# Kernel tuning notes

Hardware: AMD Instinct MI355X
Metric: run time of the kernel (lower is better)

## Reference

```python
import jax, jax.numpy as jnp
import numpy as np

EMB = 768
HEADS = 8
HEAD_DIM = EMB // HEADS  # 96
SCALING = HEAD_DIM ** -0.5


def setup_inputs() -> dict:
    key = jax.random.key(0)
    ks = jax.random.split(key, 9)
    B, S = 2, 2048
    std = 1.0 / np.sqrt(EMB)
    x = jax.random.normal(ks[0], (B, S, EMB), dtype=jnp.float32)
    # torch nn.Linear weights are [out, in]; we store [in, out] for x @ W.
    Wq = jax.random.normal(ks[1], (EMB, EMB), dtype=jnp.float32) * std
    Wk = jax.random.normal(ks[2], (EMB, EMB), dtype=jnp.float32) * std
    Wv = jax.random.normal(ks[3], (EMB, EMB), dtype=jnp.float32) * std
    Wo = jax.random.normal(ks[4], (EMB, EMB), dtype=jnp.float32) * std
    bq = jax.random.normal(ks[5], (EMB,), dtype=jnp.float32) * std
    bk = jax.random.normal(ks[6], (EMB,), dtype=jnp.float32) * std
    bv = jax.random.normal(ks[7], (EMB,), dtype=jnp.float32) * std
    bo = jax.random.normal(ks[8], (EMB,), dtype=jnp.float32) * std
    return {"x": x, "Wq": Wq, "bq": bq, "Wk": Wk, "bk": bk,
            "Wv": Wv, "bv": bv, "Wo": Wo, "bo": bo}


def _split_heads(t):
    # [B, S, E] -> [B, H, S, D]
    B, S, _ = t.shape
    return t.reshape(B, S, HEADS, HEAD_DIM).transpose(0, 2, 1, 3)


def reference(x, Wq, bq, Wk, bk, Wv, bv, Wo, bo):
    q = _split_heads(x @ Wq + bq)
    k = _split_heads(x @ Wk + bk)
    v = _split_heads(x @ Wv + bv)
    # Full [B, H, S, S] score matrix, as in the source module.
    energies = jnp.einsum('bhqd,bhkd->bhqk', q, k)
    # Faithful quirk: softmax first, THEN multiply by scaling (dropout=0 -> identity).
    attention = jax.nn.softmax(energies, axis=-1) * SCALING
    out = jnp.einsum('bhqk,bhkd->bhqd', attention, v)
    B, H, S, D = out.shape
    out = out.transpose(0, 2, 1, 3).reshape(B, S, H * D)
    return out @ Wo + bo
```

## Files before the change

### kernel.cpp

```cpp
#include <hip/hip_runtime.h>
#include <hip/hip_bf16.h>

#define EMB 768
#define HD 96
#define NH 8
#define SEQ 2048
#define SCALING 0.10206207261596575f

typedef short bf16x8 __attribute__((ext_vector_type(8)));
typedef float f32x4  __attribute__((ext_vector_type(4)));
typedef unsigned short u16v8 __attribute__((ext_vector_type(8)));
typedef unsigned short u16v4 __attribute__((ext_vector_type(4)));

union F4 { float4 v; float f[4]; };

__device__ __forceinline__ unsigned short f2bf(float v) {
    __hip_bfloat16 b = __float2bfloat16(v);
    return *reinterpret_cast<unsigned short*>(&b);
}
__device__ __forceinline__ float bf2f(unsigned short u) {
    __hip_bfloat16 b = *reinterpret_cast<__hip_bfloat16*>(&u);
    return __bfloat162float(b);
}

__device__ __forceinline__ void dma16(const unsigned short* g, unsigned short* l) {
    __builtin_amdgcn_global_load_lds(
        (const __attribute__((address_space(1))) unsigned int*)g,
        (__attribute__((address_space(3))) unsigned int*)l,
        16, 0, 0);
}

__global__ __launch_bounds__(256) void convert_x(
    const float* __restrict__ x,
    unsigned short* __restrict__ xh, unsigned short* __restrict__ xl)
{
    const size_t i0 = ((size_t)blockIdx.x * 256 + threadIdx.x) * 8;
    F4 a, b;
    a.v = *(const float4*)&x[i0];
    b.v = *(const float4*)&x[i0 + 4];
    u16v8 h, l;
    #pragma unroll
    for (int j = 0; j < 4; j++) {
        unsigned short hu = f2bf(a.f[j]);
        h[j] = hu; l[j] = f2bf(a.f[j] - bf2f(hu));
    }
    #pragma unroll
    for (int j = 0; j < 4; j++) {
        unsigned short hu = f2bf(b.f[j]);
        h[4+j] = hu; l[4+j] = f2bf(b.f[j] - bf2f(hu));
    }
    *(u16v8*)&xh[i0] = h;
    *(u16v8*)&xl[i0] = l;
}

__global__ __launch_bounds__(256) void convert_wT(
    const float* __restrict__ Wq, const float* __restrict__ Wk,
    const float* __restrict__ Wv, const float* __restrict__ Wo,
    unsigned short* __restrict__ WhT, unsigned short* __restrict__ WlT)
{
    const int z = blockIdx.z;
    const float* W = (z == 0) ? Wq : (z == 1) ? Wk : (z == 2) ? Wv : Wo;
    unsigned short* oh = WhT + (size_t)z * 589824;
    unsigned short* ol = WlT + (size_t)z * 589824;
    __shared__ float T[64][68];
    const int t = threadIdx.x;
    const int r = t >> 2, cg = (t & 3) * 16;
    const int k0 = blockIdx.x * 64, n0 = blockIdx.y * 64;
    #pragma unroll
    for (int i = 0; i < 4; i++) {
        float4 v = *(const float4*)&W[(size_t)(k0 + r) * EMB + n0 + cg + 4*i];
        *(float4*)&T[r][cg + 4*i] = v;
    }
    __syncthreads();
    #pragma unroll
    for (int i = 0; i < 4; i++) {
        u16v4 h, l;
        #pragma unroll
        for (int j = 0; j < 4; j++) {
            float v = T[cg + 4*i + j][r];
            unsigned short hu = f2bf(v);
            h[j] = hu; l[j] = f2bf(v - bf2f(hu));
        }
        *(u16v4*)&oh[(size_t)(n0 + r) * EMB + k0 + cg + 4*i] = h;
        *(u16v4*)&ol[(size_t)(n0 + r) * EMB + k0 + cg + 4*i] = l;
    }
}

#define QA_H 0
#define QA_L 4096
#define QW_H 8192
#define QW_L 12288

__global__ __launch_bounds__(256, 3) void qkv_mfma(
    const unsigned short* __restrict__ xh, const unsigned short* __restrict__ xl,
    const unsigned short* __restrict__ WhT, const unsigned short* __restrict__ WlT,
    const float* __restrict__ bq, const float* __restrict__ bk, const float* __restrict__ bv,
    unsigned short* __restrict__ Qh, unsigned short* __restrict__ Ql,
    unsigned short* __restrict__ Kb, unsigned short* __restrict__ Vt)
{
    const int which = blockIdx.z;
    const unsigned short* Wh = WhT + (size_t)which * 589824;
    const unsigned short* Wl = WlT + (size_t)which * 589824;
    const float* bias = (which == 0) ? bq : (which == 1) ? bk : bv;

    __shared__ __align__(16) unsigned short lds[16384];
    const int tid = threadIdx.x;
    const int lane = tid & 63, lo = lane & 15, h4 = lane >> 4;
    const int w = tid >> 6, wm = w & 1, wn = w >> 1;
    const int row0 = blockIdx.x * 128, col0 = blockIdx.y * 128;

    const unsigned short* sbase =
        (w == 0) ? xh + (size_t)row0 * EMB :
        (w == 1) ? xl + (size_t)row0 * EMB :
        (w == 2) ? Wh + (size_t)col0 * EMB :
                   Wl + (size_t)col0 * EMB;
    const int soff = w * 4096;

    f32x4 acc[4][4];
    #pragma unroll
    for (int i = 0; i < 4; i++)
        #pragma unroll
        for (int j = 0; j < 4; j++) acc[i][j] = (f32x4){0.f, 0.f, 0.f, 0.f};

    for (int k0 = 0; k0 < EMB; k0 += 32) {
        #pragma unroll
        for (int j = 0; j < 8; j++) {
            const int u = j*64 + lane;
            const int row = u >> 2, c8 = (u & 3) * 8;
            dma16(sbase + (size_t)row * EMB + k0 + c8, &lds[soff + j*512]);
        }
        __syncthreads();

        bf16x8 ah[4], al[4];
        #pragma unroll
        for (int i = 0; i < 4; i++)
            ah[i] = *(const bf16x8*)&lds[QA_H + (64*wm + 16*i + lo)*32 + 8*h4];
        if (which <= 1) {
            #pragma unroll
            for (int i = 0; i < 4; i++)
                al[i] = *(const bf16x8*)&lds[QA_L + (64*wm + 16*i + lo)*32 + 8*h4];
        }
        #pragma unroll
        for (int j = 0; j < 4; j++) {
            bf16x8 whf = *(const bf16x8*)&lds[QW_H + (64*wn + 16*j + lo)*32 + 8*h4];
            #pragma unroll
            for (int i = 0; i < 4; i++)
                acc[i][j] = __builtin_amdgcn_mfma_f32_16x16x32_bf16(ah[i], whf, acc[i][j], 0, 0, 0);
            if (which <= 1) {
                #pragma unroll
                for (int i = 0; i < 4; i++)
                    acc[i][j] = __builtin_amdgcn_mfma_f32_16x16x32_bf16(al[i], whf, acc[i][j], 0, 0, 0);
            }
            if (which != 1) {
                bf16x8 wlf = *(const bf16x8*)&lds[QW_L + (64*wn + 16*j + lo)*32 + 8*h4];
                #pragma unroll
                for (int i = 0; i < 4; i++)
                    acc[i][j] = __builtin_amdgcn_mfma_f32_16x16x32_bf16(ah[i], wlf, acc[i][j], 0, 0, 0);
            }
        }
        __syncthreads();
    }

    if (which == 0) {
        #pragma unroll
        for (int i = 0; i < 4; i++)
            #pragma unroll
            for (int r = 0; r < 4; r++) {
                const int sg = row0 + 64*wm + 16*i + 4*h4 + r;
                const int b = sg >> 11, s = sg & 2047;
                #pragma unroll
                for (int j = 0; j < 4; j++) {
                    const int c = col0 + 64*wn + 16*j + lo;
                    const int h = c / HD, d = c - h*HD;
                    float v = acc[i][j][r] + bias[c];
                    unsigned short hu = f2bf(v);
                    const size_t base = ((size_t)(b*NH + h) * SEQ + s) * HD + d;
                    Qh[base] = hu;
                    Ql[base] = f2bf(v - bf2f(hu));
                }
            }
    } else if (which == 1) {
        #pragma unroll
        for (int i = 0; i < 4; i++)
            #pragma unroll
            for (int r = 0; r < 4; r++) {
                const int sg = row0 + 64*wm + 16*i + 4*h4 + r;
                const int b = sg >> 11, s = sg & 2047;
                #pragma unroll
                for (int j = 0; j < 4; j++) {
                    const int c = col0 + 64*wn + 16*j + lo;
                    const int h = c / HD, d = c - h*HD;
                    float v = acc[i][j][r] + bias[c];
                    Kb[((size_t)(b*NH + h) * SEQ + s) * HD + d] = f2bf(v);
                }
            }
    } else {
        #pragma unroll
        for (int i = 0; i < 4; i++)
            #pragma unroll
            for (int r = 0; r < 4; r++) {
                const int sg = row0 + 64*wm + 16*i + 4*h4 + r;
                const int b = sg >> 11, s = sg & 2047;
                #pragma unroll
                for (int j = 0; j < 4; j++) {
                    const int c = col0 + 64*wn + 16*j + lo;
                    const int h = c / HD, d = c - h*HD;
                    float v = acc[i][j][r] + bias[c];
                    Vt[((size_t)(b*NH + h) * HD + d) * SEQ + s] = f2bf(v);
                }
            }
    }
}

#define PA_O 0
#define PWH_O 4096
#define PWL_O 6144

__global__ __launch_bounds__(256, 3) void proj_mfma(
    const unsigned short* __restrict__ AOh,
    const unsigned short* __restrict__ Wh, const unsigned short* __restrict__ Wl,
    const float* __restrict__ bo, float* __restrict__ out)
{
    __shared__ __align__(16) unsigned short lds[8192];
    const int tid = threadIdx.x;
    const int lane = tid & 63, lo = lane & 15, h4 = lane >> 4;
    const int w = tid >> 6, wm = w & 1, wn = w >> 1;
    const int row0 = blockIdx.x * 128, col0 = blockIdx.y * 64;

    const unsigned short* sbase =
        (w <= 1) ? AOh + (size_t)row0 * EMB :
        (w == 2) ? Wh  + (size_t)col0 * EMB :
                   Wl  + (size_t)col0 * EMB;
    const int jbase = (w == 1) ? 4 : 0;
    const int soff  = (w <= 1) ? PA_O : (w == 2) ? PWH_O : PWL_O;

    f32x4 acc[4][2];
    #pragma unroll
    for (int i = 0; i < 4; i++)
        #pragma unroll
        for (int j = 0; j < 2; j++) acc[i][j] = (f32x4){0.f, 0.f, 0.f, 0.f};

    for (int k0 = 0; k0 < EMB; k0 += 32) {
        #pragma unroll
        for (int jj = 0; jj < 4; jj++) {
            const int j = jbase + jj;
            const int u = j*64 + lane;
            const int row = u >> 2, c8 = (u & 3) * 8;
            dma16(sbase + (size_t)row * EMB + k0 + c8, &lds[soff + j*512]);
        }
        __syncthreads();

        bf16x8 af[4];
        #pragma unroll
        for (int i = 0; i < 4; i++)
            af[i] = *(const bf16x8*)&lds[PA_O + (64*wm + 16*i + lo)*32 + 8*h4];
        #pragma unroll
        for (int j = 0; j < 2; j++) {
            bf16x8 whf = *(const bf16x8*)&lds[PWH_O + (32*wn + 16*j + lo)*32 + 8*h4];
            bf16x8 wlf = *(const bf16x8*)&lds[PWL_O + (32*wn + 16*j + lo)*32 + 8*h4];
            #pragma unroll
            for (int i = 0; i < 4; i++) {
                acc[i][j] = __builtin_amdgcn_mfma_f32_16x16x32_bf16(af[i], whf, acc[i][j], 0, 0, 0);
                acc[i][j] = __builtin_amdgcn_mfma_f32_16x16x32_bf16(af[i], wlf, acc[i][j], 0, 0, 0);
            }
        }
        __syncthreads();
    }

    #pragma unroll
    for (int i = 0; i < 4; i++)
        #pragma unroll
        for (int r = 0; r < 4; r++) {
            const int sg = row0 + 64*wm + 16*i + 4*h4 + r;
            #pragma unroll
            for (int j = 0; j < 2; j++) {
                const int c = col0 + 32*wn + 16*j + lo;
                out[(size_t)sg * EMB + c] = acc[i][j][r] + bo[c];
            }
        }
}

__global__ __launch_bounds__(128, 2) void attn_mfma(
    const unsigned short* __restrict__ Qh, const unsigned short* __restrict__ Ql,
    const unsigned short* __restrict__ Kb, const unsigned short* __restrict__ Vt,
    unsigned short* __restrict__ AOh)
{
    __shared__ __align__(16) unsigned short lds[11072];
    const int id   = blockIdx.x;
    const int bh   = 2*(id & 7) + ((id >> 3) & 1);
    const int qb   = id >> 4;
    const int q0   = qb * 32;
    const int tid  = threadIdx.x;
    const int wk   = tid >> 6;
    const int lane = tid & 63;
    const int lo   = lane & 15;
    const int h4   = lane >> 4;

    bf16x8 qhf[2][3], qlf[2][3];
    #pragma unroll
    for (int mi = 0; mi < 2; mi++) {
        const size_t qoff = ((size_t)bh*SEQ + q0 + 16*mi + lo) * HD + 8*h4;
        #pragma unroll
        for (int ks = 0; ks < 3; ks++) {
            qhf[mi][ks] = *(const bf16x8*)&Qh[qoff + 32*ks];
            qlf[mi][ks] = *(const bf16x8*)&Ql[qoff + 32*ks];
        }
    }

    f32x4 O[2][6];
    #pragma unroll
    for (int mi = 0; mi < 2; mi++)
        #pragma unroll
        for (int i = 0; i < 6; i++) O[mi][i] = (f32x4){0.f, 0.f, 0.f, 0.f};
    float lsum[2][4] = {};

    unsigned short* Pw = lds + wk * 2304;
    const unsigned short* KbH = Kb + (size_t)bh * SEQ * HD;
    const unsigned short* VtH = Vt + (size_t)bh * HD * SEQ;

    #pragma unroll 1
    for (int c = 0; c < 16; c++) {
        const int k0 = (wk * 16 + c) * 64;
        const unsigned short* KbG = KbH + (size_t)k0 * HD;
        const unsigned short* VtG = VtH + k0;

        bf16x8 vf[2][6];
        #pragma unroll
        for (int ks2 = 0; ks2 < 2; ks2++)
            #pragma unroll
            for (int nb2 = 0; nb2 < 6; nb2++)
                vf[ks2][nb2] = *(const bf16x8*)&VtG[(size_t)(16*nb2 + lo)*SEQ + 32*ks2 + 8*h4];

        f32x4 S[2][4];
        #pragma unroll
        for (int mi = 0; mi < 2; mi++)
            #pragma unroll
            for (int nb = 0; nb < 4; nb++) S[mi][nb] = (f32x4){0.f, 0.f, 0.f, 0.f};
        #pragma unroll
        for (int ks = 0; ks < 3; ks++) {
            bf16x8 kf[4];
            #pragma unroll
            for (int nb = 0; nb < 4; nb++)
                kf[nb] = *(const bf16x8*)&KbG[(size_t)(16*nb + lo)*HD + 32*ks + 8*h4];
            #pragma unroll
            for (int nb = 0; nb < 4; nb++)
                #pragma unroll
                for (int mi = 0; mi < 2; mi++) {
                    S[mi][nb] = __builtin_amdgcn_mfma_f32_16x16x32_bf16(qhf[mi][ks], kf[nb], S[mi][nb], 0, 0, 0);
                    S[mi][nb] = __builtin_amdgcn_mfma_f32_16x16x32_bf16(qlf[mi][ks], kf[nb], S[mi][nb], 0, 0, 0);
                }
        }

        #pragma unroll
        for (int mi = 0; mi < 2; mi++)
            #pragma unroll
            for (int nb = 0; nb < 4; nb++)
                #pragma unroll
                for (int r = 0; r < 4; r++) {
                    float p = __expf(S[mi][nb][r]);
                    lsum[mi][r] += p;
                    Pw[(16*mi + 4*h4 + r)*72 + 16*nb + lo] = f2bf(p);
                }

        #pragma unroll
        for (int ks2 = 0; ks2 < 2; ks2++) {
            bf16x8 pf0 = *(const bf16x8*)&Pw[(lo)*72      + 32*ks2 + 8*h4];
            bf16x8 pf1 = *(const bf16x8*)&Pw[(16 + lo)*72 + 32*ks2 + 8*h4];
            #pragma unroll
            for (int nb2 = 0; nb2 < 6; nb2++) {
                O[0][nb2] = __builtin_amdgcn_mfma_f32_16x16x32_bf16(pf0, vf[ks2][nb2], O[0][nb2], 0, 0, 0);
                O[1][nb2] = __builtin_amdgcn_mfma_f32_16x16x32_bf16(pf1, vf[ks2][nb2], O[1][nb2], 0, 0, 0);
            }
        }
    }

    float lred[2][4];
    #pragma unroll
    for (int mi = 0; mi < 2; mi++)
        #pragma unroll
        for (int r = 0; r < 4; r++) {
            float l = lsum[mi][r];
            l += __shfl_xor(l, 1);
            l += __shfl_xor(l, 2);
            l += __shfl_xor(l, 4);
            l += __shfl_xor(l, 8);
            lred[mi][r] = l;
        }

    float* Cbuf = (float*)(lds + 4608);
    float* Lbuf = Cbuf + 3200;
    if (wk == 1) {
        #pragma unroll
        for (int mi = 0; mi < 2; mi++)
            #pragma unroll
            for (int r = 0; r < 4; r++) {
                const int row = 16*mi + 4*h4 + r;
                if (lo == 0) Lbuf[row] = lred[mi][r];
                #pragma unroll
                for (int nb2 = 0; nb2 < 6; nb2++)
                    Cbuf[row*100 + 16*nb2 + lo] = O[mi][nb2][r];
            }
    }
    __syncthreads();
    if (wk == 0) {
        const int b = bh >> 3, hh = bh & 7;
        #pragma unroll
        for (int mi = 0; mi < 2; mi++)
            #pragma unroll
            for (int r = 0; r < 4; r++) {
                const int row = 16*mi + 4*h4 + r;
                const float lt = lred[mi][r] + Lbuf[row];
                const float sc = SCALING / lt;
                const int q = q0 + row;
                const size_t base = ((size_t)b*SEQ + q)*EMB + hh*HD + lo;
                #pragma unroll
                for (int nb2 = 0; nb2 < 6; nb2++)
                    AOh[base + 16*nb2] =
                        f2bf((O[mi][nb2][r] + Cbuf[row*100 + 16*nb2 + lo]) * sc);
            }
    }
}

extern "C" void kernel_launch(void* const* d_in, const int* in_sizes, int n_in,
                              void* d_out, int out_size, void* d_ws, size_t ws_size,
                              hipStream_t stream)
{
    const float* x  = (const float*)d_in[0];
    const float* Wq = (const float*)d_in[1];
    const float* bq = (const float*)d_in[2];
    const float* Wk = (const float*)d_in[3];
    const float* bk = (const float*)d_in[4];
    const float* Wv = (const float*)d_in[5];
    const float* bv = (const float*)d_in[6];
    const float* Wo = (const float*)d_in[7];
    const float* bo = (const float*)d_in[8];
    float* out = (float*)d_out;

    unsigned short* ws = (unsigned short*)d_ws;
    const size_t HS = (size_t)16 * SEQ * HD;
    const size_t WS1 = (size_t)EMB * EMB;
    unsigned short* Qh  = ws;
    unsigned short* Ql  = ws + HS;
    unsigned short* Kb  = ws + 2*HS;
    unsigned short* Vt  = ws + 3*HS;
    unsigned short* xh  = ws + 4*HS;
    unsigned short* xl  = ws + 5*HS;
    unsigned short* WhT = ws + 6*HS;
    unsigned short* WlT = ws + 6*HS + 4*WS1;
    unsigned short* AOh = xh;

    convert_x<<<1536, 256, 0, stream>>>(x, xh, xl);
    convert_wT<<<dim3(12, 12, 4), 256, 0, stream>>>(Wq, Wk, Wv, Wo, WhT, WlT);
    qkv_mfma<<<dim3(32, 6, 3), 256, 0, stream>>>(xh, xl, WhT, WlT, bq, bk, bv,
                                                 Qh, Ql, Kb, Vt);
    attn_mfma<<<1024, 128, 0, stream>>>(Qh, Ql, Kb, Vt, AOh);
    proj_mfma<<<dim3(32, 12), 256, 0, stream>>>(AOh, WhT + 3*WS1, WlT + 3*WS1, bo, out);
}
```

Baseline: 235.4 us.

## Share K/V tiles across four query warps via double-buffered LDS staging

The attention kernel changes from 128-thread blocks of 32 queries with the key range split between two warps to 256-thread blocks where four warps each own 32 queries and sweep all keys. K and V^T tiles are staged cooperatively into padded, double-buffered LDS, with register prefetch of the next tile, instead of each warp loading its own fragments from global memory. Global K/V traffic per query drops about fourfold and the cross-warp reduction in the epilogue goes away. In exchange the grid shrinks from 1024 to 256 blocks, which is exactly one block per CU at about 72KB LDS each, and a barrier is added per key tile.

```diff
diff --git a/kernel.cpp b/kernel.cpp
--- a/kernel.cpp
+++ b/kernel.cpp
@@ -280,18 +280,24 @@
         }
 }
 
-__global__ __launch_bounds__(128, 2) void attn_mfma(
+#define AKB0 0
+#define AVB0 6656
+#define ABUF 13568
+#define AP_OFF 27136
+
+__global__ __launch_bounds__(256, 1) void attn_mfma(
     const unsigned short* __restrict__ Qh, const unsigned short* __restrict__ Ql,
     const unsigned short* __restrict__ Kb, const unsigned short* __restrict__ Vt,
     unsigned short* __restrict__ AOh)
 {
-    __shared__ __align__(16) unsigned short lds[11072];
+    __shared__ __align__(16) unsigned short lds[36352];
     const int id   = blockIdx.x;
-    const int bh   = 2*(id & 7) + ((id >> 3) & 1);
-    const int qb   = id >> 4;
-    const int q0   = qb * 32;
+    const int xcd  = id & 7;
+    const int j    = id >> 3;
+    const int bh   = 2*xcd + (j & 1);
+    const int q0   = (j >> 1) * 128;
     const int tid  = threadIdx.x;
-    const int wk   = tid >> 6;
+    const int w    = tid >> 6;
     const int lane = tid & 63;
     const int lo   = lane & 15;
     const int h4   = lane >> 4;
@@ -299,7 +305,7 @@
     bf16x8 qhf[2][3], qlf[2][3];
     #pragma unroll
     for (int mi = 0; mi < 2; mi++) {
-        const size_t qoff = ((size_t)bh*SEQ + q0 + 16*mi + lo) * HD + 8*h4;
+        const size_t qoff = ((size_t)bh*SEQ + q0 + 32*w + 16*mi + lo) * HD + 8*h4;
         #pragma unroll
         for (int ks = 0; ks < 3; ks++) {
             qhf[mi][ks] = *(const bf16x8*)&Qh[qoff + 32*ks];
@@ -314,22 +320,41 @@
         for (int i = 0; i < 6; i++) O[mi][i] = (f32x4){0.f, 0.f, 0.f, 0.f};
     float lsum[2][4] = {};
 
-    unsigned short* Pw = lds + wk * 2304;
+    unsigned short* Pw = lds + AP_OFF + w * 2304;
     const unsigned short* KbH = Kb + (size_t)bh * SEQ * HD;
     const unsigned short* VtH = Vt + (size_t)bh * HD * SEQ;
 
+    #pragma unroll
+    for (int r = 0; r < 3; r++) {
+        const int u = tid + 256*r;
+        const int kk = u / 12, g = u - kk*12;
+        *(u16v8*)&lds[AKB0 + kk*104 + 8*g] = *(const u16v8*)&KbH[kk*HD + 8*g];
+        const int dV = u >> 3, c8 = u & 7;
+        *(u16v8*)&lds[AVB0 + dV*72 + 8*c8] = *(const u16v8*)&VtH[(size_t)dV*SEQ + 8*c8];
+    }
+    __syncthreads();
+
     #pragma unroll 1
-    for (int c = 0; c < 16; c++) {
-        const int k0 = (wk * 16 + c) * 64;
-        const unsigned short* KbG = KbH + (size_t)k0 * HD;
-        const unsigned short* VtG = VtH + k0;
-
-        bf16x8 vf[2][6];
-        #pragma unroll
-        for (int ks2 = 0; ks2 < 2; ks2++)
-            #pragma unroll
-            for (int nb2 = 0; nb2 < 6; nb2++)
-                vf[ks2][nb2] = *(const bf16x8*)&VtG[(size_t)(16*nb2 + lo)*SEQ + 32*ks2 + 8*h4];
+    for (int c = 0; c < 32; c++) {
+        unsigned short* curK = lds + (c & 1) * ABUF;
+        unsigned short* curV = curK + 6656;
+        unsigned short* nxtK = lds + ((c + 1) & 1) * ABUF;
+        unsigned short* nxtV = nxtK + 6656;
+        const int kn = (c + 1 < 32) ? (c + 1) * 64 : 0;
+
+        u16v8 kst[3], vst[3];
+        {
+            const unsigned short* KG = KbH + (size_t)kn * HD;
+            const unsigned short* VG = VtH + kn;
+            #pragma unroll
+            for (int r = 0; r < 3; r++) {
+                const int u = tid + 256*r;
+                const int kk = u / 12, g = u - kk*12;
+                kst[r] = *(const u16v8*)&KG[kk*HD + 8*g];
+                const int dV = u >> 3, c8 = u & 7;
+                vst[r] = *(const u16v8*)&VG[(size_t)dV*SEQ + 8*c8];
+            }
+        }
 
         f32x4 S[2][4];
         #pragma unroll
@@ -341,7 +366,7 @@
             bf16x8 kf[4];
             #pragma unroll
             for (int nb = 0; nb < 4; nb++)
-                kf[nb] = *(const bf16x8*)&KbG[(size_t)(16*nb + lo)*HD + 32*ks + 8*h4];
+                kf[nb] = *(const bf16x8*)&curK[(16*nb + lo)*104 + 32*ks + 8*h4];
             #pragma unroll
             for (int nb = 0; nb < 4; nb++)
                 #pragma unroll
@@ -368,13 +393,24 @@
             bf16x8 pf1 = *(const bf16x8*)&Pw[(16 + lo)*72 + 32*ks2 + 8*h4];
             #pragma unroll
             for (int nb2 = 0; nb2 < 6; nb2++) {
-                O[0][nb2] = __builtin_amdgcn_mfma_f32_16x16x32_bf16(pf0, vf[ks2][nb2], O[0][nb2], 0, 0, 0);
-                O[1][nb2] = __builtin_amdgcn_mfma_f32_16x16x32_bf16(pf1, vf[ks2][nb2], O[1][nb2], 0, 0, 0);
-            }
-        }
-    }
-
-    float lred[2][4];
+                bf16x8 vfv = *(const bf16x8*)&curV[(16*nb2 + lo)*72 + 32*ks2 + 8*h4];
+                O[0][nb2] = __builtin_amdgcn_mfma_f32_16x16x32_bf16(pf0, vfv, O[0][nb2], 0, 0, 0);
+                O[1][nb2] = __builtin_amdgcn_mfma_f32_16x16x32_bf16(pf1, vfv, O[1][nb2], 0, 0, 0);
+            }
+        }
+
+        #pragma unroll
+        for (int r = 0; r < 3; r++) {
+            const int u = tid + 256*r;
+            const int kk = u / 12, g = u - kk*12;
+            *(u16v8*)&nxtK[kk*104 + 8*g] = kst[r];
+            const int dV = u >> 3, c8 = u & 7;
+            *(u16v8*)&nxtV[dV*72 + 8*c8] = vst[r];
+        }
+        __syncthreads();
+    }
+
+    const int b = bh >> 3, hh = bh & 7;
     #pragma unroll
     for (int mi = 0; mi < 2; mi++)
         #pragma unroll
@@ -384,41 +420,13 @@
             l += __shfl_xor(l, 2);
             l += __shfl_xor(l, 4);
             l += __shfl_xor(l, 8);
-            lred[mi][r] = l;
-        }
-
-    float* Cbuf = (float*)(lds + 4608);
-    float* Lbuf = Cbuf + 3200;
-    if (wk == 1) {
-        #pragma unroll
-        for (int mi = 0; mi < 2; mi++)
-            #pragma unroll
-            for (int r = 0; r < 4; r++) {
-                const int row = 16*mi + 4*h4 + r;
-                if (lo == 0) Lbuf[row] = lred[mi][r];
-                #pragma unroll
-                for (int nb2 = 0; nb2 < 6; nb2++)
-                    Cbuf[row*100 + 16*nb2 + lo] = O[mi][nb2][r];
-            }
-    }
-    __syncthreads();
-    if (wk == 0) {
-        const int b = bh >> 3, hh = bh & 7;
-        #pragma unroll
-        for (int mi = 0; mi < 2; mi++)
-            #pragma unroll
-            for (int r = 0; r < 4; r++) {
-                const int row = 16*mi + 4*h4 + r;
-                const float lt = lred[mi][r] + Lbuf[row];
-                const float sc = SCALING / lt;
-                const int q = q0 + row;
-                const size_t base = ((size_t)b*SEQ + q)*EMB + hh*HD + lo;
-                #pragma unroll
-                for (int nb2 = 0; nb2 < 6; nb2++)
-                    AOh[base + 16*nb2] =
-                        f2bf((O[mi][nb2][r] + Cbuf[row*100 + 16*nb2 + lo]) * sc);
-            }
-    }
+            const float sc = SCALING / l;
+            const int q = q0 + 32*w + 16*mi + 4*h4 + r;
+            const size_t base = ((size_t)b*SEQ + q)*EMB + hh*HD + lo;
+            #pragma unroll
+            for (int nb2 = 0; nb2 < 6; nb2++)
+                AOh[base + 16*nb2] = f2bf(O[mi][nb2][r] * sc);
+        }
 }
 
 extern "C" void kernel_launch(void* const* d_in, const int* in_sizes, int n_in,
@@ -453,6 +461,6 @@
     convert_wT<<<dim3(12, 12, 4), 256, 0, stream>>>(Wq, Wk, Wv, Wo, WhT, WlT);
     qkv_mfma<<<dim3(32, 6, 3), 256, 0, stream>>>(xh, xl, WhT, WlT, bq, bk, bv,
                                                  Qh, Ql, Kb, Vt);
-    attn_mfma<<<1024, 128, 0, stream>>>(Qh, Ql, Kb, Vt, AOh);
+    attn_mfma<<<256, 256, 0, stream>>>(Qh, Ql, Kb, Vt, AOh);
     proj_mfma<<<dim3(32, 12), 256, 0, stream>>>(AOh, WhT + 3*WS1, WlT + 3*WS1, bo, out);
 }
```

After: 216.3 us. 8.1% less time.
